# Performance work log

Hardware: AMD Instinct MI355X
Metric: run time of the kernel (lower is better)

## Reference

```python
import jax, jax.numpy as jnp
import numpy as np

N_NODES = 50000
N_EDGES = 800000
IN_CH = 128
HID = 128
OUT_CH = 64
BN_EPS = 1e-5


def setup_inputs() -> dict:
    key = jax.random.key(0)
    ks = jax.random.split(key, 12)
    glorot = lambda k, fi, fo: jax.random.normal(k, (fi, fo), jnp.float32) * np.sqrt(2.0 / (fi + fo))
    return {
        "x": jax.random.normal(ks[0], (N_NODES, IN_CH), jnp.float32),
        "edge_index": jax.random.randint(ks[1], (2, N_EDGES), 0, N_NODES, jnp.int64),
        "W1": glorot(ks[2], IN_CH, HID), "b1": jnp.zeros((HID,), jnp.float32),
        "gamma1": jnp.ones((HID,), jnp.float32), "beta1": jnp.zeros((HID,), jnp.float32),
        "W2": glorot(ks[3], HID, HID), "b2": jnp.zeros((HID,), jnp.float32),
        "gamma2": jnp.ones((HID,), jnp.float32), "beta2": jnp.zeros((HID,), jnp.float32),
        "Wmu": glorot(ks[4], HID, OUT_CH), "bmu": jnp.zeros((OUT_CH,), jnp.float32),
        "Wls": glorot(ks[5], HID, OUT_CH), "bls": jnp.zeros((OUT_CH,), jnp.float32),
    }


def _gcn(h, W, b, src, dst, norm, n):
    # GCNConv: linear transform, then normalized scatter-add aggregation
    h = h @ W                                    # [N, out]
    msg = h[src] * norm[:, None]                 # [E+N, out] gathered messages
    out = jax.ops.segment_sum(msg, dst, num_segments=n)
    return out + b


def _batch_norm(h, gamma, beta):
    mu = jnp.mean(h, axis=0)
    var = jnp.mean(jnp.square(h - mu), axis=0)   # biased var (BatchNorm1d train mode)
    return (h - mu) * jax.lax.rsqrt(var + BN_EPS) * gamma + beta


def reference(x, edge_index, W1, b1, gamma1, beta1, W2, b2, gamma2, beta2, Wmu, bmu, Wls, bls):
    n = x.shape[0]
    loops = jnp.arange(n, dtype=edge_index.dtype)
    src = jnp.concatenate([edge_index[0], loops])  # add self-loops
    dst = jnp.concatenate([edge_index[1], loops])
    # symmetric normalization deg^-1/2 A_hat deg^-1/2 (same for every layer)
    deg = jax.ops.segment_sum(jnp.ones_like(src, jnp.float32), dst, num_segments=n)
    dinv = jax.lax.rsqrt(deg)                     # deg >= 1 because of self-loops
    norm = dinv[src] * dinv[dst]

    h = jax.nn.relu(_batch_norm(_gcn(x, W1, b1, src, dst, norm, n), gamma1, beta1))
    h = jax.nn.relu(_batch_norm(_gcn(h, W2, b2, src, dst, norm, n), gamma2, beta2))
    mu = _gcn(h, Wmu, bmu, src, dst, norm, n)
    logstd = _gcn(h, Wls, bls, src, dst, norm, n)
    return (mu, logstd)
```

## Files before the change

### kernel.cpp

```cpp
#include <hip/hip_runtime.h>

#define NN 50000
#define NE 800000
#define C 128
#define OUTC 64
#define BN_EPS 1e-5f
#define INVN (1.0f / 50000.0f)
#define NBLK 49
#define NSH 8
#define SHW (NN / NSH)
#define NCHUNK 256
#define CHUNK (NE / NCHUNK)
#define FB 32

typedef __attribute__((ext_vector_type(8))) short bf16x8;
typedef __attribute__((ext_vector_type(4))) float f32x4;
typedef __attribute__((ext_vector_type(8))) unsigned short u16x8;

__device__ __forceinline__ unsigned short f2bf(float f) {
    unsigned u = __float_as_uint(f);
    u += 0x7fffu + ((u >> 16) & 1u);
    return (unsigned short)(u >> 16);
}
__device__ __forceinline__ float bf2f(unsigned short s) {
    return __uint_as_float((unsigned)s << 16);
}


__global__ __launch_bounds__(256) void pcount_kernel(const int* __restrict__ dstp, int* __restrict__ pc) {
    __shared__ int lc[8];
    int tid = threadIdx.x, mb = blockIdx.x;
    if (tid < 8) lc[tid] = 0;
    __syncthreads();
    int end = (mb + 1) * CHUNK;
    for (int e = mb * CHUNK + tid; e < end; e += 256)
        atomicAdd(&lc[dstp[e] / SHW], 1);
    __syncthreads();
    if (tid < 8) pc[mb * 8 + tid] = lc[tid];
}

__global__ __launch_bounds__(256) void pscan_kernel(const int* __restrict__ pc, int* __restrict__ po) {
    __shared__ int lds[256];
    int t = threadIdx.x;
    int v[8], s = 0;
    #pragma unroll
    for (int j = 0; j < 8; ++j) {
        int i = t * 8 + j;
        v[j] = pc[(i & (NCHUNK - 1)) * 8 + (i >> 8)];
        s += v[j];
    }
    lds[t] = s;
    __syncthreads();
    for (int off = 1; off < 256; off <<= 1) {
        int x = (t >= off) ? lds[t - off] : 0;
        __syncthreads();
        lds[t] += x;
        __syncthreads();
    }
    int excl = lds[t] - s;
    #pragma unroll
    for (int j = 0; j < 8; ++j) { po[t * 8 + j] = excl; excl += v[j]; }
}

__global__ __launch_bounds__(256) void ppart_kernel(const int* __restrict__ srcp, const int* __restrict__ dstp,
                                                    const int* __restrict__ po,
                                                    unsigned long long* __restrict__ part, int* __restrict__ cnt) {
    __shared__ int base[8], ctr[8];
    int tid = threadIdx.x, mb = blockIdx.x;
    if (tid < 8) { base[tid] = po[tid * NCHUNK + mb]; ctr[tid] = 0; }
    __syncthreads();
    int end = (mb + 1) * CHUNK;
    for (int e = mb * CHUNK + tid; e < end; e += 256) {
        int d = dstp[e], s = srcp[e];
        atomicAdd(&cnt[d], 1);
        int g = d / SHW;
        int slot = atomicAdd(&ctr[g], 1);
        part[(size_t)(base[g] + slot)] = ((unsigned long long)(unsigned)d << 32) | (unsigned)s;
    }
}

__global__ __launch_bounds__(256) void scan1_kernel(const int* __restrict__ cnt, int* __restrict__ rowptr,
                                                    float* __restrict__ dinv, int* __restrict__ bsum) {
    __shared__ int lds[256];
    int tid = threadIdx.x;
    int base = blockIdx.x * 1024 + tid * 4;
    int v[4];
    int s = 0;
    #pragma unroll
    for (int j = 0; j < 4; ++j) { int i = base + j; v[j] = (i < NN) ? cnt[i] : 0; s += v[j]; }
    lds[tid] = s;
    __syncthreads();
    for (int off = 1; off < 256; off <<= 1) {
        int x = (tid >= off) ? lds[tid - off] : 0;
        __syncthreads();
        lds[tid] += x;
        __syncthreads();
    }
    int excl = lds[tid] - s;
    #pragma unroll
    for (int j = 0; j < 4; ++j) {
        int i = base + j;
        if (i < NN) {
            rowptr[i] = excl;
            dinv[i] = rsqrtf((float)(v[j] + 1));
        }
        excl += v[j];
    }
    if (tid == 255) bsum[blockIdx.x] = lds[255];
}

__global__ __launch_bounds__(256) void scan3_kernel(const int* __restrict__ bsum, int* __restrict__ rowptr,
                                                    int* __restrict__ wpos) {
    __shared__ int boff;
    int tid = threadIdx.x;
    if (tid < 64) {
        int orig = (tid < NBLK) ? bsum[tid] : 0;
        int v = orig;
        #pragma unroll
        for (int off = 1; off < 64; off <<= 1) {
            int x = __shfl_up(v, off);
            if (tid >= off) v += x;
        }
        if (tid == (int)blockIdx.x) boff = v - orig;
    }
    __syncthreads();
    int off = boff;
    int base = blockIdx.x * 1024 + tid * 4;
    #pragma unroll
    for (int j = 0; j < 4; ++j) {
        int i = base + j;
        if (i < NN) { int r = rowptr[i] + off; rowptr[i] = r; wpos[i] = r; }
    }
    if (blockIdx.x == 0 && tid == 0) rowptr[NN] = NE;
}

__global__ __launch_bounds__(256) void fill2_kernel(const unsigned long long* __restrict__ part,
                                                    const int* __restrict__ po,
                                                    int* __restrict__ wpos, int* __restrict__ col) {
    int g = blockIdx.x & 7, ib = blockIdx.x >> 3;
    int lo = po[g * NCHUNK];
    int hi = (g == 7) ? NE : po[(g + 1) * NCHUNK];
    for (int idx = lo + ib * 256 + threadIdx.x; idx < hi; idx += FB * 256) {
        unsigned long long pk = part[idx];
        int d = (int)(pk >> 32), s = (int)(pk & 0xffffffffu);
        int p = atomicAdd(&wpos[d], 1);
        col[p] = s;
    }
}


__global__ __launch_bounds__(256) void prep_kernel(const float* __restrict__ W1, const float* __restrict__ W2,
                                                   const float* __restrict__ Wmu, const float* __restrict__ Wls,
                                                   unsigned short* __restrict__ Wpk) {
    int idx = blockIdx.x * 256 + threadIdx.x;
    if (idx >= 3 * 2048) return;
    int which = idx >> 11;
    int r = idx & 2047;
    int l = r & 63;
    int nt = (r >> 6) & 7;
    int kt = r >> 9;
    int m = l & 15, kg = l >> 4;
    int c = nt * 16 + m;
    bf16x8 o;
    #pragma unroll
    for (int j = 0; j < 8; ++j) {
        int k = kt * 32 + kg * 8 + j;
        float w;
        if (which == 0)      w = W1[k * 128 + c];
        else if (which == 1) w = W2[k * 128 + c];
        else                 w = (c < 64) ? Wmu[k * 64 + c] : Wls[k * 64 + (c - 64)];
        o[j] = (short)f2bf(w);
    }
    *(bf16x8*)&Wpk[(size_t)which * 16384 + (size_t)r * 8] = o;
}


template<bool TRANS>
__global__ __launch_bounds__(256) void gemm_kernel(
    const void* __restrict__ Av, const unsigned short* __restrict__ Wpk,
    const float* __restrict__ sums, const float* __restrict__ gamma, const float* __restrict__ beta,
    const float* __restrict__ dinv, unsigned short* __restrict__ out)
{
    int tid = threadIdx.x;
    int wv = tid >> 6, l = tid & 63;
    int m = l & 15, kg = l >> 4;
    int rhalf = wv & 1, chalf = wv >> 1;
    int row = blockIdx.x * 32 + rhalf * 16 + m;
    int rowc = min(row, NN - 1);

    f32x4 acc[4] = {};

    #pragma unroll
    for (int kt = 0; kt < 4; ++kt) {
        int k0 = kt * 32 + kg * 8;
        bf16x8 af;
        if (TRANS) {
            const unsigned short* Ar = (const unsigned short*)Av + (size_t)rowc * C;
            u16x8 raw = *(const u16x8*)&Ar[k0];
            #pragma unroll
            for (int j = 0; j < 8; ++j) {
                int k = k0 + j;
                float mean = sums[k] * INVN;
                float var = fmaf(-mean, mean, sums[128 + k] * INVN);
                float sc = gamma[k] * rsqrtf(var + BN_EPS);
                float sh = fmaf(-mean, sc, beta[k]);
                af[j] = (short)f2bf(fmaxf(fmaf(bf2f(raw[j]), sc, sh), 0.f));
            }
        } else {
            const float* Ar = (const float*)Av + (size_t)rowc * C;
            float4 x0 = *(const float4*)&Ar[k0];
            float4 x1 = *(const float4*)&Ar[k0 + 4];
            af[0] = (short)f2bf(x0.x); af[1] = (short)f2bf(x0.y);
            af[2] = (short)f2bf(x0.z); af[3] = (short)f2bf(x0.w);
            af[4] = (short)f2bf(x1.x); af[5] = (short)f2bf(x1.y);
            af[6] = (short)f2bf(x1.z); af[7] = (short)f2bf(x1.w);
        }
        #pragma unroll
        for (int n = 0; n < 4; ++n) {
            int nt = chalf * 4 + n;
            bf16x8 bfr = *(const bf16x8*)&Wpk[(size_t)((kt * 8 + nt) * 64 + l) * 8];
            acc[n] = __builtin_amdgcn_mfma_f32_16x16x32_bf16(af, bfr, acc[n], 0, 0, 0);
        }
    }

    int ro = blockIdx.x * 32 + rhalf * 16 + kg * 4;
    #pragma unroll
    for (int r = 0; r < 4; ++r) {
        int orow = ro + r;
        if (orow < NN) {
            float di = dinv[orow];
            #pragma unroll
            for (int n = 0; n < 4; ++n)
                out[(size_t)orow * C + (chalf * 4 + n) * 16 + m] = f2bf(di * acc[n][r]);
        }
    }
}


template<bool SPLIT>
__global__ __launch_bounds__(256) void agg_kernel(
    const unsigned short* __restrict__ t, const int* __restrict__ rowptr, const int* __restrict__ col,
    const float* __restrict__ dinv, const float* __restrict__ bmu, const float* __restrict__ bls,
    unsigned short* __restrict__ outb16, float* __restrict__ outmu, float* __restrict__ outls)
{
    int wave = threadIdx.x >> 6, lane = threadIdx.x & 63;
    int row = blockIdx.x * 4 + wave;
    int q = lane & 15, eg = lane >> 4;
    const unsigned short* tq = t + q * 8;
    int e0 = rowptr[row], e1 = rowptr[row + 1];
    float a[8] = {};

    for (int e = e0; e < e1; e += 16) {
        int lim = e1 - 1;
        u16x8 v[4];
        float msk[4];
        #pragma unroll
        for (int b = 0; b < 4; ++b) {
            int i = e + b * 4 + eg;
            msk[b] = (i < e1) ? 1.f : 0.f;
            if (e + b * 4 < e1) {
                int s = col[min(i, lim)];
                v[b] = *(const u16x8*)&tq[(size_t)s * C];
            } else {
                v[b] = (u16x8)0;
                msk[b] = 0.f;
            }
        }
        #pragma unroll
        for (int b = 0; b < 4; ++b) {
            #pragma unroll
            for (int j = 0; j < 8; ++j)
                a[j] = fmaf(msk[b], bf2f(v[b][j]), a[j]);
        }
    }

    {
        u16x8 vs = *(const u16x8*)&tq[(size_t)row * C];
        float ms = (eg == 0) ? 1.f : 0.f;
        #pragma unroll
        for (int j = 0; j < 8; ++j)
            a[j] = fmaf(ms, bf2f(vs[j]), a[j]);
    }

    #pragma unroll
    for (int j = 0; j < 8; ++j) {
        a[j] += __shfl_xor(a[j], 16);
        a[j] += __shfl_xor(a[j], 32);
    }

    if (eg == 0) {
        float di = dinv[row];
        int c = q * 8;
        if (!SPLIT) {
            u16x8 o;
            #pragma unroll
            for (int j = 0; j < 8; ++j) o[j] = f2bf(di * a[j]);
            *(u16x8*)&outb16[(size_t)row * C + c] = o;
        } else {
            if (c < 64) {
                float4 b0 = *(const float4*)&bmu[c];
                float4 b1 = *(const float4*)&bmu[c + 4];
                *(float4*)&outmu[(size_t)row * OUTC + c]
                    = make_float4(fmaf(di,a[0],b0.x), fmaf(di,a[1],b0.y), fmaf(di,a[2],b0.z), fmaf(di,a[3],b0.w));
                *(float4*)&outmu[(size_t)row * OUTC + c + 4]
                    = make_float4(fmaf(di,a[4],b1.x), fmaf(di,a[5],b1.y), fmaf(di,a[6],b1.z), fmaf(di,a[7],b1.w));
            } else {
                int cc = c - 64;
                float4 b0 = *(const float4*)&bls[cc];
                float4 b1 = *(const float4*)&bls[cc + 4];
                *(float4*)&outls[(size_t)row * OUTC + cc]
                    = make_float4(fmaf(di,a[0],b0.x), fmaf(di,a[1],b0.y), fmaf(di,a[2],b0.z), fmaf(di,a[3],b0.w));
                *(float4*)&outls[(size_t)row * OUTC + cc + 4]
                    = make_float4(fmaf(di,a[4],b1.x), fmaf(di,a[5],b1.y), fmaf(di,a[6],b1.z), fmaf(di,a[7],b1.w));
            }
        }
    }
}


__global__ __launch_bounds__(256) void bnstats_kernel(const unsigned short* __restrict__ h, float* __restrict__ sums) {
    int c = threadIdx.x & 127;
    int hh = threadIdx.x >> 7;
    float s = 0.f, sq = 0.f;
    for (int r = blockIdx.x * 2 + hh; r < NN; r += gridDim.x * 2) {
        float v = bf2f(h[(size_t)r * C + c]);
        s += v; sq = fmaf(v, v, sq);
    }
    __shared__ float ls[256], lq[256];
    ls[threadIdx.x] = s; lq[threadIdx.x] = sq;
    __syncthreads();
    if (hh == 0) {
        atomicAdd(&sums[c], s + ls[c + 128]);
        atomicAdd(&sums[128 + c], sq + lq[c + 128]);
    }
}


extern "C" void kernel_launch(void* const* d_in, const int* in_sizes, int n_in,
                              void* d_out, int out_size, void* d_ws, size_t ws_size,
                              hipStream_t stream) {
    (void)in_sizes; (void)n_in; (void)out_size; (void)ws_size;
    const float* x      = (const float*)d_in[0];
    const int*   ei     = (const int*)d_in[1];
    const float* W1     = (const float*)d_in[2];
    const float* gamma1 = (const float*)d_in[4];
    const float* beta1  = (const float*)d_in[5];
    const float* W2     = (const float*)d_in[6];
    const float* gamma2 = (const float*)d_in[8];
    const float* beta2  = (const float*)d_in[9];
    const float* Wmu    = (const float*)d_in[10];
    const float* bmu    = (const float*)d_in[11];
    const float* Wls    = (const float*)d_in[12];
    const float* bls    = (const float*)d_in[13];

    float* outmu = (float*)d_out;
    float* outls = outmu + (size_t)NN * OUTC;

    char* w = (char*)d_ws;
    size_t off = 0;
    auto alloc = [&](size_t bytes) { char* p = w + off; off = (off + bytes + 255) & ~(size_t)255; return p; };
    unsigned short* t    = (unsigned short*)alloc(sizeof(unsigned short) * NN * C);
    unsigned short* aggb = (unsigned short*)alloc(sizeof(unsigned short) * NN * C);
    int*   cnt    = (int*)  alloc(sizeof(int) * NN);
    float* sums   = (float*)alloc(sizeof(float) * 512);
    int*   rowptr = (int*)  alloc(sizeof(int) * (NN + 1));
    int*   wpos   = (int*)  alloc(sizeof(int) * NN);
    int*   col    = (int*)  alloc(sizeof(int) * NE);
    float* dinv   = (float*)alloc(sizeof(float) * NN);
    int*   bsum   = (int*)  alloc(sizeof(int) * 64);
    int*   pc     = (int*)  alloc(sizeof(int) * NCHUNK * 8);
    int*   po     = (int*)  alloc(sizeof(int) * NCHUNK * 8);
    unsigned long long* part = (unsigned long long*)alloc(sizeof(unsigned long long) * NE);
    unsigned short* Wpk = (unsigned short*)alloc(sizeof(unsigned short) * 3 * 16384);
    float* sumsA = sums; float* sumsB = sums + 256;

    const int* srcp = ei;
    const int* dstp = ei + NE;

    size_t zspan = (size_t)((char*)(sums + 512) - (char*)cnt);
    hipMemsetAsync(cnt, 0, zspan, stream);

    pcount_kernel<<<NCHUNK, 256, 0, stream>>>(dstp, pc);
    pscan_kernel<<<1, 256, 0, stream>>>(pc, po);
    ppart_kernel<<<NCHUNK, 256, 0, stream>>>(srcp, dstp, po, part, cnt);
    scan1_kernel<<<NBLK, 256, 0, stream>>>(cnt, rowptr, dinv, bsum);
    scan3_kernel<<<NBLK, 256, 0, stream>>>(bsum, rowptr, wpos);
    fill2_kernel<<<NSH * FB, 256, 0, stream>>>(part, po, wpos, col);
    prep_kernel<<<24, 256, 0, stream>>>(W1, W2, Wmu, Wls, Wpk);

    const int GB = (NN + 31) / 32;
    const int AB = NN / 4;

    gemm_kernel<false><<<GB, 256, 0, stream>>>(x, Wpk, nullptr, nullptr, nullptr, dinv, t);
    agg_kernel<false><<<AB, 256, 0, stream>>>(t, rowptr, col, dinv, nullptr, nullptr, aggb, nullptr, nullptr);
    bnstats_kernel<<<400, 256, 0, stream>>>(aggb, sumsA);

    gemm_kernel<true><<<GB, 256, 0, stream>>>(aggb, Wpk + 16384, sumsA, gamma1, beta1, dinv, t);
    agg_kernel<false><<<AB, 256, 0, stream>>>(t, rowptr, col, dinv, nullptr, nullptr, aggb, nullptr, nullptr);
    bnstats_kernel<<<400, 256, 0, stream>>>(aggb, sumsB);

    gemm_kernel<true><<<GB, 256, 0, stream>>>(aggb, Wpk + 32768, sumsB, gamma2, beta2, dinv, t);
    agg_kernel<true><<<AB, 256, 0, stream>>>(t, rowptr, col, dinv, bmu, bls, nullptr, outmu, outls);
}
```

Before: 397.2 us.

## Precompute BN scale/shift, vectorize bnstats, localize degree counting, widen agg unroll

Several independent changes. The per-destination degree atomics move out of the partition kernel into a separate kernel that walks the shard-partitioned edge list, so atomics hit a localized node range. BatchNorm statistics now use 16-byte vector loads with an LDS reduction across a smaller grid, and a tiny finalize kernel precomputes per-channel scale and shift so the GEMM no longer recomputes rsqrt per element. The aggregation loop gathers 32 edges per iteration instead of 16 to keep more loads in flight, at the cost of more registers and two extra launches.

```diff
diff --git a/kernel.cpp b/kernel.cpp
--- a/kernel.cpp
+++ b/kernel.cpp
@@ -64,7 +64,7 @@
 
 __global__ __launch_bounds__(256) void ppart_kernel(const int* __restrict__ srcp, const int* __restrict__ dstp,
                                                     const int* __restrict__ po,
-                                                    unsigned long long* __restrict__ part, int* __restrict__ cnt) {
+                                                    unsigned long long* __restrict__ part) {
     __shared__ int base[8], ctr[8];
     int tid = threadIdx.x, mb = blockIdx.x;
     if (tid < 8) { base[tid] = po[tid * NCHUNK + mb]; ctr[tid] = 0; }
@@ -72,11 +72,19 @@
     int end = (mb + 1) * CHUNK;
     for (int e = mb * CHUNK + tid; e < end; e += 256) {
         int d = dstp[e], s = srcp[e];
-        atomicAdd(&cnt[d], 1);
         int g = d / SHW;
         int slot = atomicAdd(&ctr[g], 1);
         part[(size_t)(base[g] + slot)] = ((unsigned long long)(unsigned)d << 32) | (unsigned)s;
     }
+}
+
+__global__ __launch_bounds__(256) void cntloc_kernel(const unsigned long long* __restrict__ part,
+                                                     const int* __restrict__ po, int* __restrict__ cnt) {
+    int g = blockIdx.x & 7, ib = blockIdx.x >> 3;
+    int lo = po[g * NCHUNK];
+    int hi = (g == 7) ? NE : po[(g + 1) * NCHUNK];
+    for (int idx = lo + ib * 256 + threadIdx.x; idx < hi; idx += FB * 256)
+        atomicAdd(&cnt[(int)(part[idx] >> 32)], 1);
 }
 
 __global__ __launch_bounds__(256) void scan1_kernel(const int* __restrict__ cnt, int* __restrict__ rowptr,
@@ -178,7 +186,7 @@
 template<bool TRANS>
 __global__ __launch_bounds__(256) void gemm_kernel(
     const void* __restrict__ Av, const unsigned short* __restrict__ Wpk,
-    const float* __restrict__ sums, const float* __restrict__ gamma, const float* __restrict__ beta,
+    const float* __restrict__ scale, const float* __restrict__ shift,
     const float* __restrict__ dinv, unsigned short* __restrict__ out)
 {
     int tid = threadIdx.x;
@@ -197,15 +205,15 @@
         if (TRANS) {
             const unsigned short* Ar = (const unsigned short*)Av + (size_t)rowc * C;
             u16x8 raw = *(const u16x8*)&Ar[k0];
+            float4 sc0 = *(const float4*)&scale[k0];
+            float4 sc1 = *(const float4*)&scale[k0 + 4];
+            float4 sh0 = *(const float4*)&shift[k0];
+            float4 sh1 = *(const float4*)&shift[k0 + 4];
+            float scv[8] = {sc0.x, sc0.y, sc0.z, sc0.w, sc1.x, sc1.y, sc1.z, sc1.w};
+            float shv[8] = {sh0.x, sh0.y, sh0.z, sh0.w, sh1.x, sh1.y, sh1.z, sh1.w};
             #pragma unroll
-            for (int j = 0; j < 8; ++j) {
-                int k = k0 + j;
-                float mean = sums[k] * INVN;
-                float var = fmaf(-mean, mean, sums[128 + k] * INVN);
-                float sc = gamma[k] * rsqrtf(var + BN_EPS);
-                float sh = fmaf(-mean, sc, beta[k]);
-                af[j] = (short)f2bf(fmaxf(fmaf(bf2f(raw[j]), sc, sh), 0.f));
-            }
+            for (int j = 0; j < 8; ++j)
+                af[j] = (short)f2bf(fmaxf(fmaf(bf2f(raw[j]), scv[j], shv[j]), 0.f));
         } else {
             const float* Ar = (const float*)Av + (size_t)rowc * C;
             float4 x0 = *(const float4*)&Ar[k0];
@@ -250,24 +258,24 @@
     int e0 = rowptr[row], e1 = rowptr[row + 1];
     float a[8] = {};
 
-    for (int e = e0; e < e1; e += 16) {
+    for (int e = e0; e < e1; e += 32) {
         int lim = e1 - 1;
-        u16x8 v[4];
-        float msk[4];
-        #pragma unroll
-        for (int b = 0; b < 4; ++b) {
+        u16x8 v[8];
+        float msk[8];
+        #pragma unroll
+        for (int b = 0; b < 8; ++b) {
             int i = e + b * 4 + eg;
-            msk[b] = (i < e1) ? 1.f : 0.f;
             if (e + b * 4 < e1) {
                 int s = col[min(i, lim)];
                 v[b] = *(const u16x8*)&tq[(size_t)s * C];
+                msk[b] = (i < e1) ? 1.f : 0.f;
             } else {
                 v[b] = (u16x8)0;
                 msk[b] = 0.f;
             }
         }
         #pragma unroll
-        for (int b = 0; b < 4; ++b) {
+        for (int b = 0; b < 8; ++b) {
             #pragma unroll
             for (int j = 0; j < 8; ++j)
                 a[j] = fmaf(msk[b], bf2f(v[b][j]), a[j]);
@@ -319,20 +327,45 @@
 
 
 __global__ __launch_bounds__(256) void bnstats_kernel(const unsigned short* __restrict__ h, float* __restrict__ sums) {
-    int c = threadIdx.x & 127;
-    int hh = threadIdx.x >> 7;
-    float s = 0.f, sq = 0.f;
-    for (int r = blockIdx.x * 2 + hh; r < NN; r += gridDim.x * 2) {
-        float v = bf2f(h[(size_t)r * C + c]);
-        s += v; sq = fmaf(v, v, sq);
-    }
-    __shared__ float ls[256], lq[256];
-    ls[threadIdx.x] = s; lq[threadIdx.x] = sq;
-    __syncthreads();
-    if (hh == 0) {
-        atomicAdd(&sums[c], s + ls[c + 128]);
-        atomicAdd(&sums[128 + c], sq + lq[c + 128]);
-    }
+    __shared__ float ls[16][128], lq[16][128];
+    int c8 = threadIdx.x & 15, rs = threadIdx.x >> 4;
+    float s[8] = {}, sq[8] = {};
+    for (int r = blockIdx.x * 16 + rs; r < NN; r += gridDim.x * 16) {
+        u16x8 v = *(const u16x8*)&h[(size_t)r * C + c8 * 8];
+        #pragma unroll
+        for (int j = 0; j < 8; ++j) {
+            float f = bf2f(v[j]);
+            s[j] += f; sq[j] = fmaf(f, f, sq[j]);
+        }
+    }
+    #pragma unroll
+    for (int j = 0; j < 8; ++j) { ls[rs][c8 * 8 + j] = s[j]; lq[rs][c8 * 8 + j] = sq[j]; }
+    __syncthreads();
+    int tid = threadIdx.x;
+    if (tid < 128) {
+        float acc = 0.f;
+        #pragma unroll
+        for (int p = 0; p < 16; ++p) acc += ls[p][tid];
+        atomicAdd(&sums[tid], acc);
+    } else {
+        int c = tid - 128;
+        float acc = 0.f;
+        #pragma unroll
+        for (int p = 0; p < 16; ++p) acc += lq[p][c];
+        atomicAdd(&sums[128 + c], acc);
+    }
+}
+
+
+__global__ __launch_bounds__(128) void bnfin_kernel(const float* __restrict__ sums,
+                                                    const float* __restrict__ gamma, const float* __restrict__ beta,
+                                                    float* __restrict__ scale, float* __restrict__ shift) {
+    int c = threadIdx.x;
+    float mean = sums[c] * INVN;
+    float var = fmaf(-mean, mean, sums[128 + c] * INVN);
+    float s = gamma[c] * rsqrtf(var + BN_EPS);
+    scale[c] = s;
+    shift[c] = fmaf(-mean, s, beta[c]);
 }
 
 
@@ -372,6 +405,10 @@
     int*   po     = (int*)  alloc(sizeof(int) * NCHUNK * 8);
     unsigned long long* part = (unsigned long long*)alloc(sizeof(unsigned long long) * NE);
     unsigned short* Wpk = (unsigned short*)alloc(sizeof(unsigned short) * 3 * 16384);
+    float* scale1 = (float*)alloc(512);
+    float* shift1 = (float*)alloc(512);
+    float* scale2 = (float*)alloc(512);
+    float* shift2 = (float*)alloc(512);
     float* sumsA = sums; float* sumsB = sums + 256;
 
     const int* srcp = ei;
@@ -382,7 +419,8 @@
 
     pcount_kernel<<<NCHUNK, 256, 0, stream>>>(dstp, pc);
     pscan_kernel<<<1, 256, 0, stream>>>(pc, po);
-    ppart_kernel<<<NCHUNK, 256, 0, stream>>>(srcp, dstp, po, part, cnt);
+    ppart_kernel<<<NCHUNK, 256, 0, stream>>>(srcp, dstp, po, part);
+    cntloc_kernel<<<NSH * FB, 256, 0, stream>>>(part, po, cnt);
     scan1_kernel<<<NBLK, 256, 0, stream>>>(cnt, rowptr, dinv, bsum);
     scan3_kernel<<<NBLK, 256, 0, stream>>>(bsum, rowptr, wpos);
     fill2_kernel<<<NSH * FB, 256, 0, stream>>>(part, po, wpos, col);
@@ -391,14 +429,16 @@
     const int GB = (NN + 31) / 32;
     const int AB = NN / 4;
 
-    gemm_kernel<false><<<GB, 256, 0, stream>>>(x, Wpk, nullptr, nullptr, nullptr, dinv, t);
+    gemm_kernel<false><<<GB, 256, 0, stream>>>(x, Wpk, nullptr, nullptr, dinv, t);
     agg_kernel<false><<<AB, 256, 0, stream>>>(t, rowptr, col, dinv, nullptr, nullptr, aggb, nullptr, nullptr);
-    bnstats_kernel<<<400, 256, 0, stream>>>(aggb, sumsA);
-
-    gemm_kernel<true><<<GB, 256, 0, stream>>>(aggb, Wpk + 16384, sumsA, gamma1, beta1, dinv, t);
+    bnstats_kernel<<<100, 256, 0, stream>>>(aggb, sumsA);
+    bnfin_kernel<<<1, 128, 0, stream>>>(sumsA, gamma1, beta1, scale1, shift1);
+
+    gemm_kernel<true><<<GB, 256, 0, stream>>>(aggb, Wpk + 16384, scale1, shift1, dinv, t);
     agg_kernel<false><<<AB, 256, 0, stream>>>(t, rowptr, col, dinv, nullptr, nullptr, aggb, nullptr, nullptr);
-    bnstats_kernel<<<400, 256, 0, stream>>>(aggb, sumsB);
-
-    gemm_kernel<true><<<GB, 256, 0, stream>>>(aggb, Wpk + 32768, sumsB, gamma2, beta2, dinv, t);
+    bnstats_kernel<<<100, 256, 0, stream>>>(aggb, sumsB);
+    bnfin_kernel<<<1, 128, 0, stream>>>(sumsB, gamma2, beta2, scale2, shift2);
+
+    gemm_kernel<true><<<GB, 256, 0, stream>>>(aggb, Wpk + 32768, scale2, shift2, dinv, t);
     agg_kernel<true><<<AB, 256, 0, stream>>>(t, rowptr, col, dinv, bmu, bls, nullptr, outmu, outls);
 }
```

Result: faster. 373.9 us (-5.9%).
